# Performance work log

Measured on AMD Instinct MI355X. Metric: run time of the kernel, lower is better.

Reference implementation:

```python
import jax, jax.numpy as jnp
import numpy as np

B, L, H, U = 4, 1024, 16, 64  # batch, length, num_heads, units (per-head dim)
D_IN = 1024                   # input feature dim
D_MODEL = H * U               # 1024


def setup_inputs() -> dict:
    key = jax.random.key(0)
    ks = jax.random.split(key, 12)
    s_in = 1.0 / np.sqrt(D_IN)
    s_md = 1.0 / np.sqrt(D_MODEL)
    return {
        "v": jax.random.normal(ks[0], (B, L, D_IN), jnp.float32),
        "k": jax.random.normal(ks[1], (B, L, D_IN), jnp.float32),
        "q": jax.random.normal(ks[2], (B, L, D_IN), jnp.float32),
        "wq": jax.random.normal(ks[3], (D_IN, D_MODEL), jnp.float32) * s_in,
        "bq": jnp.zeros((D_MODEL,), jnp.float32),
        "wk": jax.random.normal(ks[4], (D_IN, D_MODEL), jnp.float32) * s_in,
        "bk": jnp.zeros((D_MODEL,), jnp.float32),
        "wv": jax.random.normal(ks[5], (D_IN, D_MODEL), jnp.float32) * s_in,
        "bv": jnp.zeros((D_MODEL,), jnp.float32),
        "wo": jax.random.normal(ks[6], (D_MODEL, U), jnp.float32) * s_md,  # dense: units*num_heads -> units
        "bo": jnp.zeros((U,), jnp.float32),
    }


def _split_heads(x):
    # (B, L, H*U) -> (B, H, L, U)
    return x.reshape(B, L, H, U).transpose(0, 2, 1, 3)


def reference(v, k, q, wq, bq, wk, bk, wv, bv, wo, bo):
    qh = _split_heads(q @ wq + bq)
    kh = _split_heads(k @ wk + bk)
    vh = _split_heads(v @ wv + bv)
    scale = 1.0 / jnp.sqrt(jnp.asarray(U, jnp.float32))
    logits = jnp.einsum("bhqd,bhkd->bhqk", qh, kh) * scale
    attn = jax.nn.softmax(logits, axis=-1)  # (B, H, Lq, Lk)
    ctx = jnp.einsum("bhqk,bhkd->bhqd", attn, vh)
    concat = ctx.transpose(0, 2, 1, 3).reshape(B, L, D_MODEL)
    out = concat @ wo + bo  # (B, L, U)
    return out, attn
```

## Files before the change

kernel.cpp:

```cpp
#include <hip/hip_runtime.h>
#include <hip/hip_bf16.h>


typedef __attribute__((ext_vector_type(8))) short s8v;
typedef __attribute__((ext_vector_type(4))) float f4v;

#define MFMA16(a, b, c) __builtin_amdgcn_mfma_f32_16x16x32_bf16(a, b, c, 0, 0, 0)

__device__ __forceinline__ ushort f2bf(float x) {
    unsigned u = __float_as_uint(x);
    return (ushort)((u + 0x7FFF + ((u >> 16) & 1)) >> 16);
}
__device__ __forceinline__ void split2(float x, ushort& h, ushort& l) {
    h = f2bf(x);
    float hf = __uint_as_float(((unsigned)h) << 16);
    l = f2bf(x - hf);
}

__global__ __launch_bounds__(256) void pack_wt(const float* __restrict__ W,
                                               ushort* __restrict__ Wt_hi,
                                               ushort* __restrict__ Wt_lo) {
    __shared__ float tile[32][36];
    const int t = threadIdx.x;
    const int n0 = blockIdx.x * 32, k0 = blockIdx.y * 32;
    {
        const int kr = t >> 3, c4 = (t & 7) * 4;
        float4 v = *(const float4*)&W[(size_t)(k0 + kr) * 1024 + n0 + c4];
        *(float4*)&tile[kr][c4] = v;
    }
    __syncthreads();
    {
        const int n = t >> 3, k4 = (t & 7) * 4;
        ushort4 h, l;
        split2(tile[k4 + 0][n], h.x, l.x);
        split2(tile[k4 + 1][n], h.y, l.y);
        split2(tile[k4 + 2][n], h.z, l.z);
        split2(tile[k4 + 3][n], h.w, l.w);
        *(ushort4*)&Wt_hi[(size_t)(n0 + n) * 1024 + k0 + k4] = h;
        *(ushort4*)&Wt_lo[(size_t)(n0 + n) * 1024 + k0 + k4] = l;
    }
}

#define PROJ_LDSTRIDE 40
template <bool SPLIT>
__global__ __launch_bounds__(256, 2) void gemm_proj_mfma(
    const float* __restrict__ X, const ushort* __restrict__ Wt_hi,
    const ushort* __restrict__ Wt_lo, const float* __restrict__ bias,
    ushort* __restrict__ Yhi, ushort* __restrict__ Ylo) {
    __shared__ ushort As_hi[128 * PROJ_LDSTRIDE];
    __shared__ ushort As_lo[128 * PROJ_LDSTRIDE];
    __shared__ ushort Bs_hi[128 * PROJ_LDSTRIDE];
    __shared__ ushort Bs_lo[128 * PROJ_LDSTRIDE];

    const int t = threadIdx.x;
    const int lane = t & 63, w = t >> 6;
    const int wm = (w & 1) * 64, wn = (w >> 1) * 64;
    const int fr = lane & 15, q8 = (lane >> 4) * 8;
    const int row0 = blockIdx.y * 128, col0 = blockIdx.x * 128;

    const int srow = t >> 1, skb = (t & 1) * 16;

    f4v acc[4][4] = {};

    for (int k0 = 0; k0 < 1024; k0 += 32) {
        {
            const float* xp = &X[(size_t)(row0 + srow) * 1024 + k0 + skb];
#pragma unroll
            for (int j = 0; j < 4; ++j) {
                float4 x4 = *(const float4*)&xp[4 * j];
                ushort4 h, l;
                split2(x4.x, h.x, l.x);
                split2(x4.y, h.y, l.y);
                split2(x4.z, h.z, l.z);
                split2(x4.w, h.w, l.w);
                *(ushort4*)&As_hi[srow * PROJ_LDSTRIDE + skb + 4 * j] = h;
                if (SPLIT) *(ushort4*)&As_lo[srow * PROJ_LDSTRIDE + skb + 4 * j] = l;
            }
        }
        {
            const ushort* bp = &Wt_hi[(size_t)(col0 + srow) * 1024 + k0 + skb];
            *(uint4*)&Bs_hi[srow * PROJ_LDSTRIDE + skb] = *(const uint4*)bp;
            *(uint4*)&Bs_hi[srow * PROJ_LDSTRIDE + skb + 8] = *(const uint4*)(bp + 8);
            if (SPLIT) {
                const ushort* bl = &Wt_lo[(size_t)(col0 + srow) * 1024 + k0 + skb];
                *(uint4*)&Bs_lo[srow * PROJ_LDSTRIDE + skb] = *(const uint4*)bl;
                *(uint4*)&Bs_lo[srow * PROJ_LDSTRIDE + skb + 8] = *(const uint4*)(bl + 8);
            }
        }
        __syncthreads();

        s8v a_hi[4], a_lo[4], b_hi[4], b_lo[4];
#pragma unroll
        for (int mi = 0; mi < 4; ++mi) {
            a_hi[mi] = *(const s8v*)&As_hi[(wm + mi * 16 + fr) * PROJ_LDSTRIDE + q8];
            if (SPLIT) a_lo[mi] = *(const s8v*)&As_lo[(wm + mi * 16 + fr) * PROJ_LDSTRIDE + q8];
        }
#pragma unroll
        for (int ni = 0; ni < 4; ++ni) {
            b_hi[ni] = *(const s8v*)&Bs_hi[(wn + ni * 16 + fr) * PROJ_LDSTRIDE + q8];
            if (SPLIT) b_lo[ni] = *(const s8v*)&Bs_lo[(wn + ni * 16 + fr) * PROJ_LDSTRIDE + q8];
        }
#pragma unroll
        for (int mi = 0; mi < 4; ++mi)
#pragma unroll
            for (int ni = 0; ni < 4; ++ni) {
                acc[mi][ni] = MFMA16(a_hi[mi], b_hi[ni], acc[mi][ni]);
                if (SPLIT) {
                    acc[mi][ni] = MFMA16(a_hi[mi], b_lo[ni], acc[mi][ni]);
                    acc[mi][ni] = MFMA16(a_lo[mi], b_hi[ni], acc[mi][ni]);
                }
            }
        __syncthreads();
    }

#pragma unroll
    for (int mi = 0; mi < 4; ++mi)
#pragma unroll
        for (int ni = 0; ni < 4; ++ni)
#pragma unroll
            for (int r = 0; r < 4; ++r) {
                const int lr = wm + mi * 16 + (lane >> 4) * 4 + r;
                const int lc = wn + ni * 16 + fr;
                const int grow = row0 + lr;
                const int b = grow >> 10, ll = grow & 1023;
                const int gcol = col0 + lc;
                const int h = gcol >> 6, u = gcol & 63;
                const float val = acc[mi][ni][r] + bias[gcol];
                const size_t o = ((size_t)((b * 16 + h) * 1024 + ll)) * 64 + u;
                if (SPLIT) {
                    ushort hh, lll;
                    split2(val, hh, lll);
                    Yhi[o] = hh;
                    Ylo[o] = lll;
                } else {
                    Yhi[o] = f2bf(val);
                }
            }
}

__global__ __launch_bounds__(256) void trans_vh(const ushort* __restrict__ vh,
                                                ushort* __restrict__ vhT) {
    __shared__ ushort st[64][72];
    const int t = threadIdx.x;
    const int bh = blockIdx.y, l0 = blockIdx.x * 64;
    {
        const int l = t >> 2, uc = (t & 3) * 16;
        const ushort* src = &vh[((size_t)bh * 1024 + l0 + l) * 64 + uc];
        *(uint4*)&st[l][uc] = *(const uint4*)src;
        *(uint4*)&st[l][uc + 8] = *(const uint4*)(src + 8);
    }
    __syncthreads();
    {
        const int u = t >> 2, lc = (t & 3) * 16;
        ushort tmp[16];
#pragma unroll
        for (int i = 0; i < 16; ++i) tmp[i] = st[lc + i][u];
        ushort* dst = &vhT[((size_t)bh * 64 + u) * 1024 + l0 + lc];
        *(uint4*)dst = *(uint4*)&tmp[0];
        *(uint4*)(dst + 8) = *(uint4*)&tmp[8];
    }
}

__device__ __forceinline__ int swz(int row, int c) {
    return row * 1024 + ((((c >> 2) ^ (row & 7)) << 2) | (c & 3));
}

__global__ __launch_bounds__(256, 2) void attn_fused(
    const ushort* __restrict__ qh_hi, const ushort* __restrict__ qh_lo,
    const ushort* __restrict__ kh_hi, const ushort* __restrict__ kh_lo,
    const ushort* __restrict__ vhT, float* __restrict__ attn,
    float* __restrict__ ctx) {
    __shared__ float probs[16 * 1024];

    const int t = threadIdx.x, lane = t & 63, w = t >> 6;
    const int bh = blockIdx.y, q0 = blockIdx.x * 16;
    const int fr = lane & 15, q8 = (lane >> 4) * 8;
    const size_t hbase = (size_t)bh * 1024 * 64;

    const ushort* qp = &qh_hi[hbase + (size_t)(q0 + fr) * 64];
    const ushort* ql = &qh_lo[hbase + (size_t)(q0 + fr) * 64];
    const s8v qa_h0 = *(const s8v*)(qp + q8), qa_h1 = *(const s8v*)(qp + 32 + q8);
    const s8v qa_l0 = *(const s8v*)(ql + q8), qa_l1 = *(const s8v*)(ql + 32 + q8);

    for (int i = 0; i < 16; ++i) {
        const int nt = w + i * 4;
        const ushort* kp = &kh_hi[hbase + (size_t)(nt * 16 + fr) * 64];
        const ushort* kl = &kh_lo[hbase + (size_t)(nt * 16 + fr) * 64];
        const s8v kb_h0 = *(const s8v*)(kp + q8), kb_h1 = *(const s8v*)(kp + 32 + q8);
        const s8v kb_l0 = *(const s8v*)(kl + q8), kb_l1 = *(const s8v*)(kl + 32 + q8);
        f4v a0 = {}, a1 = {}, a2 = {};
        a0 = MFMA16(qa_h0, kb_h0, a0);
        a0 = MFMA16(qa_h1, kb_h1, a0);
        a1 = MFMA16(qa_h0, kb_l0, a1);
        a1 = MFMA16(qa_h1, kb_l1, a1);
        a2 = MFMA16(qa_l0, kb_h0, a2);
        a2 = MFMA16(qa_l1, kb_h1, a2);
#pragma unroll
        for (int r = 0; r < 4; ++r) {
            const int row = (lane >> 4) * 4 + r;
            const int c = nt * 16 + fr;
            probs[swz(row, c)] = (a0[r] + a1[r] + a2[r]) * 0.125f;
        }
    }
    __syncthreads();

    for (int rr = 0; rr < 4; ++rr) {
        const int row = w * 4 + rr;
        float v[16];
#pragma unroll
        for (int j = 0; j < 16; ++j) v[j] = probs[swz(row, lane + j * 64)];
        float m = v[0];
#pragma unroll
        for (int j = 1; j < 16; ++j) m = fmaxf(m, v[j]);
        for (int off = 32; off > 0; off >>= 1) m = fmaxf(m, __shfl_xor(m, off));
        float s = 0.f;
#pragma unroll
        for (int j = 0; j < 16; ++j) {
            v[j] = __expf(v[j] - m);
            s += v[j];
        }
        for (int off = 32; off > 0; off >>= 1) s += __shfl_xor(s, off);
        const float inv = 1.0f / s;
        float* arow = &attn[((size_t)bh << 20) + (size_t)(q0 + row) * 1024];
#pragma unroll
        for (int j = 0; j < 16; ++j) {
            const float p = v[j] * inv;
            probs[swz(row, lane + j * 64)] = p;
            arow[lane + j * 64] = p;
        }
    }
    __syncthreads();

    f4v cacc = {};
    const ushort* vp = &vhT[hbase + (size_t)(w * 16 + fr) * 1024];
    for (int ks = 0; ks < 32; ++ks) {
        const int k0 = ks * 32 + q8;
        const float4 pa = *(const float4*)&probs[swz(fr, k0)];
        const float4 pb = *(const float4*)&probs[swz(fr, k0 + 4)];
        s8v a;
        a[0] = (short)f2bf(pa.x); a[1] = (short)f2bf(pa.y);
        a[2] = (short)f2bf(pa.z); a[3] = (short)f2bf(pa.w);
        a[4] = (short)f2bf(pb.x); a[5] = (short)f2bf(pb.y);
        a[6] = (short)f2bf(pb.z); a[7] = (short)f2bf(pb.w);
        const s8v b = *(const s8v*)(vp + ks * 32 + q8);
        cacc = MFMA16(a, b, cacc);
    }
#pragma unroll
    for (int r = 0; r < 4; ++r) {
        const int row = (lane >> 4) * 4 + r;
        ctx[((size_t)bh * 1024 + q0 + row) * 64 + w * 16 + fr] = cacc[r];
    }
}

#define LDS_PAD 68
__global__ __launch_bounds__(256) void gemm_out(const float* __restrict__ ctx,
                                                const float* __restrict__ wo,
                                                const float* __restrict__ bo,
                                                float* __restrict__ out) {
    __shared__ float As[16][LDS_PAD];
    __shared__ float Bs[16][LDS_PAD];
    const int t = threadIdx.x;
    const int tx = t & 15, ty = t >> 4;
    const int row0 = blockIdx.y * 64;

    const int am = t >> 2, ak4 = t & 3;
    const int bk = t >> 4, bn4 = t & 15;

    float acc[4][4] = {};
    for (int k0 = 0; k0 < 1024; k0 += 16) {
        const int r = row0 + am;
        const int b = r >> 10, l = r & 1023;
        const int c = k0 + ak4 * 4;
        const int h = c >> 6, d = c & 63;
        float4 a = *(const float4*)&ctx[(size_t)((b * 16 + h) * 1024 + l) * 64 + d];
        float4 bvv = *(const float4*)&wo[(size_t)(k0 + bk) * 64 + bn4 * 4];
        As[ak4 * 4 + 0][am] = a.x; As[ak4 * 4 + 1][am] = a.y;
        As[ak4 * 4 + 2][am] = a.z; As[ak4 * 4 + 3][am] = a.w;
        Bs[bk][bn4 * 4 + 0] = bvv.x; Bs[bk][bn4 * 4 + 1] = bvv.y;
        Bs[bk][bn4 * 4 + 2] = bvv.z; Bs[bk][bn4 * 4 + 3] = bvv.w;
        __syncthreads();
#pragma unroll
        for (int kk = 0; kk < 16; ++kk) {
            float av[4], bv[4];
#pragma unroll
            for (int i = 0; i < 4; ++i) av[i] = As[kk][ty * 4 + i];
#pragma unroll
            for (int j = 0; j < 4; ++j) bv[j] = Bs[kk][tx * 4 + j];
#pragma unroll
            for (int i = 0; i < 4; ++i)
#pragma unroll
                for (int j = 0; j < 4; ++j) acc[i][j] += av[i] * bv[j];
        }
        __syncthreads();
    }
#pragma unroll
    for (int i = 0; i < 4; ++i) {
        const int r = row0 + ty * 4 + i;
#pragma unroll
        for (int j = 0; j < 4; ++j) {
            const int u = tx * 4 + j;
            out[(size_t)r * 64 + u] = acc[i][j] + bo[u];
        }
    }
}

extern "C" void kernel_launch(void* const* d_in, const int* in_sizes, int n_in,
                              void* d_out, int out_size, void* d_ws, size_t ws_size,
                              hipStream_t stream) {
    const float* v_in = (const float*)d_in[0];
    const float* k_in = (const float*)d_in[1];
    const float* q_in = (const float*)d_in[2];
    const float* wq = (const float*)d_in[3];
    const float* bq = (const float*)d_in[4];
    const float* wk = (const float*)d_in[5];
    const float* bk = (const float*)d_in[6];
    const float* wv = (const float*)d_in[7];
    const float* bv = (const float*)d_in[8];
    const float* wo = (const float*)d_in[9];
    const float* bo = (const float*)d_in[10];

    float* out = (float*)d_out;
    float* attn = out + 262144;

    char* w8 = (char*)d_ws;
    const size_t MB = 1u << 20;
    ushort* wtq_hi = (ushort*)(w8 + 0 * MB);
    ushort* wtq_lo = (ushort*)(w8 + 2 * MB);
    ushort* wtk_hi = (ushort*)(w8 + 4 * MB);
    ushort* wtk_lo = (ushort*)(w8 + 6 * MB);
    ushort* wtv_hi = (ushort*)(w8 + 8 * MB);
    ushort* wtv_lo = (ushort*)(w8 + 10 * MB);
    ushort* qh_hi = (ushort*)(w8 + 12 * MB);
    ushort* qh_lo = (ushort*)(w8 + 20 * MB);
    ushort* kh_hi = (ushort*)(w8 + 28 * MB);
    ushort* kh_lo = (ushort*)(w8 + 36 * MB);
    ushort* vh_hi = (ushort*)(w8 + 44 * MB);
    ushort* vh_lo = (ushort*)(w8 + 52 * MB);
    ushort* vhT = (ushort*)(w8 + 60 * MB);
    float* ctx = (float*)(w8 + 68 * MB);

    dim3 blk(256);
    pack_wt<<<dim3(32, 32), blk, 0, stream>>>(wq, wtq_hi, wtq_lo);
    pack_wt<<<dim3(32, 32), blk, 0, stream>>>(wk, wtk_hi, wtk_lo);
    pack_wt<<<dim3(32, 32), blk, 0, stream>>>(wv, wtv_hi, wtv_lo);

    gemm_proj_mfma<true><<<dim3(8, 32), blk, 0, stream>>>(q_in, wtq_hi, wtq_lo, bq, qh_hi, qh_lo);
    gemm_proj_mfma<true><<<dim3(8, 32), blk, 0, stream>>>(k_in, wtk_hi, wtk_lo, bk, kh_hi, kh_lo);
    gemm_proj_mfma<false><<<dim3(8, 32), blk, 0, stream>>>(v_in, wtv_hi, wtv_lo, bv, vh_hi, vh_lo);

    trans_vh<<<dim3(16, 64), blk, 0, stream>>>(vh_hi, vhT);

    attn_fused<<<dim3(64, 64), blk, 0, stream>>>(qh_hi, qh_lo, kh_hi, kh_lo, vhT, attn, ctx);

    gemm_out<<<dim3(1, 64), blk, 0, stream>>>(ctx, wo, bo, out);
}
```

Measured before the change: 741.0 us.

## Keep attention logits in registers and stage bf16 probabilities in LDS

The attention kernel now keeps the QK^T logits in registers and runs the softmax max and sum reductions through shuffles plus a small LDS reduction across waves, so the fp32 probability tile no longer round-trips through shared memory. Probabilities are stored to LDS as bf16 with a new XOR swizzle, which halves LDS use (from 64KB to 32KB) and allows a launch bound of 4 blocks per CU. The attn output is written with nontemporal stores, and the grid is flattened with a remapping that interleaves block ids across XCDs. The cost is more register pressure from the 64-float logits array, and the extra occupancy may not be reached if registers spill.

```diff
diff --git a/kernel.cpp b/kernel.cpp
--- a/kernel.cpp
+++ b/kernel.cpp
@@ -161,20 +161,25 @@
     }
 }
 
-__device__ __forceinline__ int swz(int row, int c) {
-    return row * 1024 + ((((c >> 2) ^ (row & 7)) << 2) | (c & 3));
-}
-
-__global__ __launch_bounds__(256, 2) void attn_fused(
+
+__device__ __forceinline__ int pswz(int row, int b) {
+    return row * 2048 + (b ^ ((row & 7) << 4) ^ ((row & 8) << 2));
+}
+
+__global__ __launch_bounds__(256, 4) void attn_fused(
     const ushort* __restrict__ qh_hi, const ushort* __restrict__ qh_lo,
     const ushort* __restrict__ kh_hi, const ushort* __restrict__ kh_lo,
     const ushort* __restrict__ vhT, float* __restrict__ attn,
     float* __restrict__ ctx) {
-    __shared__ float probs[16 * 1024];
+    __shared__ ushort Pl[16 * 1024];
+    __shared__ float redA[4][16];
+    __shared__ float redB[4][16];
 
     const int t = threadIdx.x, lane = t & 63, w = t >> 6;
-    const int bh = blockIdx.y, q0 = blockIdx.x * 16;
-    const int fr = lane & 15, q8 = (lane >> 4) * 8;
+    const int bid = blockIdx.x;
+    const int sbid = (bid & 7) * 512 + (bid >> 3);
+    const int bh = sbid >> 6, q0 = (sbid & 63) * 16;
+    const int fr = lane & 15, g = lane >> 4, q8 = g * 8;
     const size_t hbase = (size_t)bh * 1024 * 64;
 
     const ushort* qp = &qh_hi[hbase + (size_t)(q0 + fr) * 64];
@@ -182,6 +187,8 @@
     const s8v qa_h0 = *(const s8v*)(qp + q8), qa_h1 = *(const s8v*)(qp + 32 + q8);
     const s8v qa_l0 = *(const s8v*)(ql + q8), qa_l1 = *(const s8v*)(ql + 32 + q8);
 
+    f4v lg[16];
+#pragma unroll
     for (int i = 0; i < 16; ++i) {
         const int nt = w + i * 4;
         const ushort* kp = &kh_hi[hbase + (size_t)(nt * 16 + fr) * 64];
@@ -196,60 +203,84 @@
         a2 = MFMA16(qa_l0, kb_h0, a2);
         a2 = MFMA16(qa_l1, kb_h1, a2);
 #pragma unroll
+        for (int r = 0; r < 4; ++r) lg[i][r] = (a0[r] + a1[r] + a2[r]) * 0.125f;
+    }
+
+    float mx[4];
+#pragma unroll
+    for (int r = 0; r < 4; ++r) {
+        float m = lg[0][r];
+#pragma unroll
+        for (int i = 1; i < 16; ++i) m = fmaxf(m, lg[i][r]);
+        m = fmaxf(m, __shfl_xor(m, 1));
+        m = fmaxf(m, __shfl_xor(m, 2));
+        m = fmaxf(m, __shfl_xor(m, 4));
+        m = fmaxf(m, __shfl_xor(m, 8));
+        mx[r] = m;
+    }
+    if (fr == 0) {
+#pragma unroll
+        for (int r = 0; r < 4; ++r) redA[w][4 * g + r] = mx[r];
+    }
+    __syncthreads();
+    float m4[4];
+#pragma unroll
+    for (int r = 0; r < 4; ++r)
+        m4[r] = fmaxf(fmaxf(redA[0][4 * g + r], redA[1][4 * g + r]),
+                      fmaxf(redA[2][4 * g + r], redA[3][4 * g + r]));
+
+    float sm[4] = {0.f, 0.f, 0.f, 0.f};
+#pragma unroll
+    for (int i = 0; i < 16; ++i)
+#pragma unroll
         for (int r = 0; r < 4; ++r) {
-            const int row = (lane >> 4) * 4 + r;
-            const int c = nt * 16 + fr;
-            probs[swz(row, c)] = (a0[r] + a1[r] + a2[r]) * 0.125f;
-        }
-    }
-    __syncthreads();
-
-    for (int rr = 0; rr < 4; ++rr) {
-        const int row = w * 4 + rr;
-        float v[16];
-#pragma unroll
-        for (int j = 0; j < 16; ++j) v[j] = probs[swz(row, lane + j * 64)];
-        float m = v[0];
-#pragma unroll
-        for (int j = 1; j < 16; ++j) m = fmaxf(m, v[j]);
-        for (int off = 32; off > 0; off >>= 1) m = fmaxf(m, __shfl_xor(m, off));
-        float s = 0.f;
-#pragma unroll
-        for (int j = 0; j < 16; ++j) {
-            v[j] = __expf(v[j] - m);
-            s += v[j];
-        }
-        for (int off = 32; off > 0; off >>= 1) s += __shfl_xor(s, off);
-        const float inv = 1.0f / s;
-        float* arow = &attn[((size_t)bh << 20) + (size_t)(q0 + row) * 1024];
-#pragma unroll
-        for (int j = 0; j < 16; ++j) {
-            const float p = v[j] * inv;
-            probs[swz(row, lane + j * 64)] = p;
-            arow[lane + j * 64] = p;
+            const float e = __expf(lg[i][r] - m4[r]);
+            lg[i][r] = e;
+            sm[r] += e;
+        }
+#pragma unroll
+    for (int r = 0; r < 4; ++r) {
+        sm[r] += __shfl_xor(sm[r], 1);
+        sm[r] += __shfl_xor(sm[r], 2);
+        sm[r] += __shfl_xor(sm[r], 4);
+        sm[r] += __shfl_xor(sm[r], 8);
+    }
+    if (fr == 0) {
+#pragma unroll
+        for (int r = 0; r < 4; ++r) redB[w][4 * g + r] = sm[r];
+    }
+    __syncthreads();
+    float inv[4];
+#pragma unroll
+    for (int r = 0; r < 4; ++r)
+        inv[r] = 1.0f / (redB[0][4 * g + r] + redB[1][4 * g + r] +
+                         redB[2][4 * g + r] + redB[3][4 * g + r]);
+
+    char* Pb = (char*)Pl;
+    float* abase = attn + ((size_t)bh << 20) + (size_t)(q0 + 4 * g) * 1024 + fr;
+#pragma unroll
+    for (int i = 0; i < 16; ++i) {
+        const int nt = w + i * 4;
+#pragma unroll
+        for (int r = 0; r < 4; ++r) {
+            const float p = lg[i][r] * inv[r];
+            __builtin_nontemporal_store(p, abase + (size_t)r * 1024 + nt * 16);
+            *(ushort*)(Pb + pswz(4 * g + r, (nt * 16 + fr) * 2)) = f2bf(p);
         }
     }
     __syncthreads();
 
     f4v cacc = {};
     const ushort* vp = &vhT[hbase + (size_t)(w * 16 + fr) * 1024];
+#pragma unroll 4
     for (int ks = 0; ks < 32; ++ks) {
-        const int k0 = ks * 32 + q8;
-        const float4 pa = *(const float4*)&probs[swz(fr, k0)];
-        const float4 pb = *(const float4*)&probs[swz(fr, k0 + 4)];
-        s8v a;
-        a[0] = (short)f2bf(pa.x); a[1] = (short)f2bf(pa.y);
-        a[2] = (short)f2bf(pa.z); a[3] = (short)f2bf(pa.w);
-        a[4] = (short)f2bf(pb.x); a[5] = (short)f2bf(pb.y);
-        a[6] = (short)f2bf(pb.z); a[7] = (short)f2bf(pb.w);
+        const s8v a = *(const s8v*)(Pb + pswz(fr, ks * 64 + q8 * 2));
         const s8v b = *(const s8v*)(vp + ks * 32 + q8);
         cacc = MFMA16(a, b, cacc);
     }
 #pragma unroll
-    for (int r = 0; r < 4; ++r) {
-        const int row = (lane >> 4) * 4 + r;
-        ctx[((size_t)bh * 1024 + q0 + row) * 64 + w * 16 + fr] = cacc[r];
-    }
+    for (int r = 0; r < 4; ++r)
+        ctx[((size_t)bh * 1024 + q0 + 4 * g + r) * 64 + w * 16 + fr] = cacc[r];
 }
 
 #define LDS_PAD 68
@@ -350,7 +381,7 @@
 
     trans_vh<<<dim3(16, 64), blk, 0, stream>>>(vh_hi, vhT);
 
-    attn_fused<<<dim3(64, 64), blk, 0, stream>>>(qh_hi, qh_lo, kh_hi, kh_lo, vhT, attn, ctx);
+    attn_fused<<<dim3(4096), blk, 0, stream>>>(qh_hi, qh_lo, kh_hi, kh_lo, vhT, attn, ctx);
 
     gemm_out<<<dim3(1, 64), blk, 0, stream>>>(ctx, wo, bo, out);
 }
```

Result: no change. 732.2 us (-1.2%).
